# Performance work log

Measured on AMD Instinct MI355X. Metric: run time of the kernel, lower is better.

## Reference

```python
import jax, jax.numpy as jnp
import numpy as np

N = 100000
E = 2000000
F = 64          # in_features == out_features (required by attention * h_j)
BETA = 0.5
NEG_SLOPE = 0.01  # torch F.leaky_relu default


def setup_inputs() -> dict:
    key = jax.random.key(0)
    k1, k2, k3, k4, k5, k6 = jax.random.split(key, 6)
    h = jax.random.normal(k1, (N, F), dtype=jnp.float32)
    adj = jax.random.randint(k2, (2, E), 0, N, dtype=jnp.int64)
    amount = jax.random.uniform(k3, (E,), dtype=jnp.float32)
    count = jax.random.uniform(k4, (E,), dtype=jnp.float32)
    fc_w = jax.random.normal(k5, (F, 2 * F), dtype=jnp.float32) * (1.0 / np.sqrt(2 * F))
    fc_b = jax.random.normal(k6, (F,), dtype=jnp.float32) * 0.01
    return {"h": h, "adj": adj, "amount": amount, "count": count,
            "fc_w": fc_w, "fc_b": fc_b}


def _minmax_norm(x):
    lo, hi = x.min(), x.max()
    return (x - lo) / (hi - lo + 1e-8)


def reference(h, adj, amount, count, fc_w, fc_b):
    # per-edge weight from normalized amount/count
    edge_weight = BETA * _minmax_norm(amount) + (1.0 - BETA) * _minmax_norm(count)  # [E]

    src, dst = adj[0], adj[1]
    h_i = h[src]                     # [E, F]
    h_j = h[dst]                     # [E, F]
    h_cat = jnp.concatenate([h_i, h_j], axis=1)  # [E, 2F]

    score = jnp.einsum('ef,of->eo', h_cat, fc_w) + fc_b  # [E, F_out]
    score = jnp.where(score >= 0, score, NEG_SLOPE * score)  # leaky_relu
    score = score * edge_weight[:, None]

    # softmax over ALL edges (dim 0), per feature, as in the original
    attention = jax.nn.softmax(score, axis=0)  # [E, F]

    agg = jnp.zeros_like(h).at[src].add(attention * h_j)  # scatter-add -> [N, F]
    return agg
```

## Files before the change

kernel.cpp:

```cpp
#include <hip/hip_runtime.h>
#include <hip/hip_fp16.h>
#include <math.h>

#define FDIM   64
#define NB     64
#define BSHIFT 7
#define BMASK  127
#define EPTA   16
#define CHUNKA (EPTA * 256)
#define SCH    1024
#define DMASK  0xFFFFF

__global__ __launch_bounds__(256) void count_mm_k(const int* __restrict__ src,
                                                  const float* __restrict__ amount,
                                                  const float* __restrict__ count,
                                                  int* __restrict__ mat,
                                                  float4* __restrict__ partial,
                                                  double* __restrict__ colsum,
                                                  int E, int nblkA, int nbkt) {
  __shared__ int lhist[1024];
  __shared__ float4 lred[4];
  for (int k = threadIdx.x; k < nbkt; k += 256) lhist[k] = 0;
  if (blockIdx.x == 0)
    for (int i = threadIdx.x; i < 1024; i += 256) colsum[i] = 0.0;
  __syncthreads();
  float amin = 3.4e38f, amax = -3.4e38f, cmin = 3.4e38f, cmax = -3.4e38f;
  int e0 = blockIdx.x * CHUNKA + threadIdx.x * EPTA;
  if (e0 + EPTA <= E) {
    #pragma unroll
    for (int q = 0; q < EPTA; q += 4) {
      int4   s4 = *(const int4*)(src + e0 + q);
      float4 a4 = *(const float4*)(amount + e0 + q);
      float4 c4 = *(const float4*)(count + e0 + q);
      atomicAdd(&lhist[s4.x >> BSHIFT], 1);
      atomicAdd(&lhist[s4.y >> BSHIFT], 1);
      atomicAdd(&lhist[s4.z >> BSHIFT], 1);
      atomicAdd(&lhist[s4.w >> BSHIFT], 1);
      amin = fminf(amin, fminf(fminf(a4.x, a4.y), fminf(a4.z, a4.w)));
      amax = fmaxf(amax, fmaxf(fmaxf(a4.x, a4.y), fmaxf(a4.z, a4.w)));
      cmin = fminf(cmin, fminf(fminf(c4.x, c4.y), fminf(c4.z, c4.w)));
      cmax = fmaxf(cmax, fmaxf(fmaxf(c4.x, c4.y), fmaxf(c4.z, c4.w)));
    }
  } else {
    for (int e = e0; e < E; e++) {
      atomicAdd(&lhist[src[e] >> BSHIFT], 1);
      float a = amount[e], c = count[e];
      amin = fminf(amin, a); amax = fmaxf(amax, a);
      cmin = fminf(cmin, c); cmax = fmaxf(cmax, c);
    }
  }
  #pragma unroll
  for (int off = 32; off; off >>= 1) {
    amin = fminf(amin, __shfl_down(amin, off));
    amax = fmaxf(amax, __shfl_down(amax, off));
    cmin = fminf(cmin, __shfl_down(cmin, off));
    cmax = fmaxf(cmax, __shfl_down(cmax, off));
  }
  if ((threadIdx.x & 63) == 0) lred[threadIdx.x >> 6] = make_float4(amin, amax, cmin, cmax);
  __syncthreads();
  for (int k = threadIdx.x; k < nbkt; k += 256)
    mat[(size_t)k * nblkA + blockIdx.x] = lhist[k];
  if (threadIdx.x == 0) {
    float4 r = lred[0];
    #pragma unroll
    for (int w = 1; w < 4; w++) {
      r.x = fminf(r.x, lred[w].x); r.y = fmaxf(r.y, lred[w].y);
      r.z = fminf(r.z, lred[w].z); r.w = fmaxf(r.w, lred[w].w);
    }
    partial[blockIdx.x] = r;
  }
}

__global__ __launch_bounds__(256) void scan1_k(const int* __restrict__ v,
                                               int* __restrict__ bsum, int M) {
  __shared__ int lds[256];
  int t = threadIdx.x, b = blockIdx.x;
  int s = 0;
  for (int i = b * SCH + t; i < min((b + 1) * SCH, M); i += 256) s += v[i];
  lds[t] = s; __syncthreads();
  for (int off = 128; off; off >>= 1) {
    if (t < off) lds[t] += lds[t + off];
    __syncthreads();
  }
  if (t == 0) bsum[b] = lds[0];
}

__global__ __launch_bounds__(256) void scan2_k(const int* __restrict__ bsum,
                                               int* __restrict__ bexcl, int nchunk,
                                               const float4* __restrict__ partial,
                                               float* __restrict__ mmf, int nb) {
  __shared__ int lds[256];
  int t = threadIdx.x;
  int running = 0;
  for (int c0 = 0; c0 < nchunk; c0 += 256) {
    int x = (c0 + t < nchunk) ? bsum[c0 + t] : 0;
    lds[t] = x; __syncthreads();
    for (int off = 1; off < 256; off <<= 1) {
      int v = (t >= off) ? lds[t - off] : 0;
      __syncthreads();
      lds[t] += v; __syncthreads();
    }
    if (c0 + t < nchunk) bexcl[c0 + t] = running + lds[t] - x;
    running += lds[255];
    __syncthreads();
  }
  float amin = 3.4e38f, amax = -3.4e38f, cmin = 3.4e38f, cmax = -3.4e38f;
  for (int i = t; i < nb; i += 256) {
    float4 p = partial[i];
    amin = fminf(amin, p.x); amax = fmaxf(amax, p.y);
    cmin = fminf(cmin, p.z); cmax = fmaxf(cmax, p.w);
  }
  #pragma unroll
  for (int off = 32; off; off >>= 1) {
    amin = fminf(amin, __shfl_down(amin, off));
    amax = fmaxf(amax, __shfl_down(amax, off));
    cmin = fminf(cmin, __shfl_down(cmin, off));
    cmax = fmaxf(cmax, __shfl_down(cmax, off));
  }
  __shared__ float4 lred[4];
  if ((t & 63) == 0) lred[t >> 6] = make_float4(amin, amax, cmin, cmax);
  __syncthreads();
  if (t == 0) {
    float4 r = lred[0];
    #pragma unroll
    for (int w = 1; w < 4; w++) {
      r.x = fminf(r.x, lred[w].x); r.y = fmaxf(r.y, lred[w].y);
      r.z = fminf(r.z, lred[w].z); r.w = fmaxf(r.w, lred[w].w);
    }
    mmf[0] = r.x; mmf[1] = r.y; mmf[2] = r.z; mmf[3] = r.w;
  }
}

__global__ __launch_bounds__(256) void scan3_k(const int* __restrict__ v,
                                               const int* __restrict__ bexcl,
                                               int* __restrict__ smat, int M) {
  __shared__ int lds[256];
  int t = threadIdx.x, b = blockIdx.x;
  int running = bexcl[b];
  for (int tile = 0; tile < SCH; tile += 256) {
    int i = b * SCH + tile + t;
    int x = (i < M) ? v[i] : 0;
    lds[t] = x; __syncthreads();
    for (int off = 1; off < 256; off <<= 1) {
      int vv = (t >= off) ? lds[t - off] : 0;
      __syncthreads();
      lds[t] += vv; __syncthreads();
    }
    if (i < M) smat[i] = running + lds[t] - x;
    running += lds[255];
    __syncthreads();
  }
}

__global__ __launch_bounds__(256) void scatter_k(const int* __restrict__ src,
                                                 const int* __restrict__ dst,
                                                 const float* __restrict__ amount,
                                                 const float* __restrict__ count,
                                                 const float* __restrict__ mmf,
                                                 const int* __restrict__ smat,
                                                 int2* __restrict__ payload,
                                                 int E, int nblkA, int nbkt) {
  __shared__ int cntb[1024];
  __shared__ int baseb[1024];
  __shared__ int sbase[1024];
  __shared__ int wsum[4];
  __shared__ int2 lpay[CHUNKA];
  __shared__ unsigned short lbkt[CHUNKA];
  const int t = threadIdx.x, blk = blockIdx.x;
  for (int k = t; k < nbkt; k += 256) {
    cntb[k] = 0;
    sbase[k] = smat[(size_t)k * nblkA + blk];
  }
  __syncthreads();
  const float amin = mmf[0], amax = mmf[1], cmin = mmf[2], cmax = mmf[3];
  const float L2E = 1.4426950408889634f;
  const float ascale = 0.5f * L2E / (amax - amin + 1e-8f);
  const float cscale = 0.5f * L2E / (cmax - cmin + 1e-8f);
  int e0 = blk * CHUNKA + t * EPTA;
  const bool full = (e0 + EPTA <= E);
  int4 S[4]; int4 D[4]; float4 A[4]; float4 C[4];
  if (full) {
    #pragma unroll
    for (int q = 0; q < 4; q++) {
      S[q] = *(const int4*)(src + e0 + 4 * q);
      D[q] = *(const int4*)(dst + e0 + 4 * q);
      A[q] = *(const float4*)(amount + e0 + 4 * q);
      C[q] = *(const float4*)(count + e0 + 4 * q);
      atomicAdd(&cntb[S[q].x >> BSHIFT], 1);
      atomicAdd(&cntb[S[q].y >> BSHIFT], 1);
      atomicAdd(&cntb[S[q].z >> BSHIFT], 1);
      atomicAdd(&cntb[S[q].w >> BSHIFT], 1);
    }
  } else {
    for (int e = e0; e < E; e++) atomicAdd(&cntb[src[e] >> BSHIFT], 1);
  }
  __syncthreads();
  {
    const int wv = t >> 6, ln = t & 63;
    int carry = 0;
    #pragma unroll
    for (int c = 0; c < 4; c++) {
      int idx = (wv << 8) + (c << 6) + ln;
      int x = (idx < nbkt) ? cntb[idx] : 0;
      int v = x;
      #pragma unroll
      for (int off = 1; off < 64; off <<= 1) {
        int u = __shfl_up(v, off);
        if (ln >= off) v += u;
      }
      if (idx < nbkt) baseb[idx] = carry + v - x;
      carry += __shfl(v, 63);
    }
    if (ln == 0) wsum[wv] = carry;
  }
  __syncthreads();
  {
    const int wv = t >> 6, ln = t & 63;
    int wpre = 0;
    #pragma unroll
    for (int i = 0; i < 4; i++) wpre += (i < wv) ? wsum[i] : 0;
    if (wpre) {
      #pragma unroll
      for (int c = 0; c < 4; c++) {
        int idx = (wv << 8) + (c << 6) + ln;
        if (idx < nbkt) baseb[idx] += wpre;
      }
    }
  }
  __syncthreads();
  for (int k = t; k < nbkt; k += 256) cntb[k] = baseb[k];
  __syncthreads();
  auto ins = [&](int s, int d, float a, float c) {
    int b = s >> BSHIFT;
    float ew = (a - amin) * ascale + (c - cmin) * cscale;
    int pos = atomicAdd(&cntb[b], 1);
    lpay[pos] = make_int2(d | ((s & BMASK) << 20), __float_as_int(ew));
    lbkt[pos] = (unsigned short)b;
  };
  if (full) {
    #pragma unroll
    for (int q = 0; q < 4; q++) {
      ins(S[q].x, D[q].x, A[q].x, C[q].x);
      ins(S[q].y, D[q].y, A[q].y, C[q].y);
      ins(S[q].z, D[q].z, A[q].z, C[q].z);
      ins(S[q].w, D[q].w, A[q].w, C[q].w);
    }
  } else {
    for (int e = e0; e < E; e++) ins(src[e], dst[e], amount[e], count[e]);
  }
  __syncthreads();
  const int ned = min(CHUNKA, E - blk * CHUNKA);
  for (int i = t; i < ned; i += 256) {
    int bk = lbkt[i];
    payload[sbase[bk] + (i - baseb[bk])] = lpay[i];
  }
}

__global__ __launch_bounds__(512) void binB_k(const int2* __restrict__ payload,
                                              const int* __restrict__ smat,
                                              int2* __restrict__ edge_s,
                                              int E, int nblkA, int nbkt) {
  __shared__ int fcnt[128];
  __shared__ int fs[128];
  __shared__ int fcur[128];
  const int b = blockIdx.x;
  const int t = threadIdx.x;
  const int base = smat[(size_t)b * nblkA];
  const int end  = (b + 1 < nbkt) ? smat[(size_t)(b + 1) * nblkA] : E;
  if (t < 128) fcnt[t] = 0;
  __syncthreads();
  for (int i = base + t; i < end; i += 512)
    atomicAdd(&fcnt[payload[i].x >> 20], 1);
  __syncthreads();
  if (t < 128) fs[t] = fcnt[t];
  __syncthreads();
  for (int off = 1; off < 128; off <<= 1) {
    int v = 0;
    if (t < 128 && t >= off) v = fs[t - off];
    __syncthreads();
    if (t < 128) fs[t] += v;
    __syncthreads();
  }
  if (t < 128) fcur[t] = base + fs[t] - fcnt[t];
  __syncthreads();
  for (int i = base + t; i < end; i += 512) {
    int2 v = payload[i];
    int pos = atomicAdd(&fcur[v.x >> 20], 1);
    edge_s[pos] = v;
  }
}

__global__ __launch_bounds__(128) void pre_gemm(const float* __restrict__ h,
                                                const float* __restrict__ fc_w,
                                                const float* __restrict__ fc_b,
                                                float* __restrict__ G1,
                                                __half2* __restrict__ P, int N) {
  __shared__ float hs[NB * FDIM];
  const int t = threadIdx.x;
  const int o = t & 63, half = t >> 6;
  float w[FDIM];
  const float* wrow = fc_w + o * 128 + half * 64;
  #pragma unroll
  for (int f = 0; f < FDIM; f += 4) {
    float4 v = *(const float4*)(wrow + f);
    w[f] = v.x; w[f + 1] = v.y; w[f + 2] = v.z; w[f + 3] = v.w;
  }
  const float bias = (half == 0) ? fc_b[o] : 0.0f;
  const int n0 = blockIdx.x * NB;
  const int nrows = min(NB, N - n0);
  for (int i = t; i < nrows * FDIM; i += 128) hs[i] = h[(size_t)n0 * FDIM + i];
  __syncthreads();
  for (int n = 0; n < nrows; n++) {
    float4 a4 = make_float4(0.f, 0.f, 0.f, 0.f);
    #pragma unroll
    for (int f = 0; f < FDIM; f += 4) {
      float4 hv = *(const float4*)(&hs[n * FDIM + f]);
      a4.x += hv.x * w[f];
      a4.y += hv.y * w[f + 1];
      a4.z += hv.z * w[f + 2];
      a4.w += hv.w * w[f + 3];
    }
    float acc = (a4.x + a4.y) + (a4.z + a4.w) + bias;
    if (half == 0) {
      G1[(size_t)(n0 + n) * FDIM + o] = acc;
    } else {
      P[(size_t)(n0 + n) * FDIM + o] =
          __halves2half2(__float2half(acc), __float2half(hs[n * FDIM + o]));
    }
  }
}

__device__ __forceinline__ float2 unpack_h2(unsigned u) {
  __half2 v = *(__half2*)&u;
  return make_float2(__low2float(v), __high2float(v));
}

__global__ __launch_bounds__(256) void fused_k(const int2* __restrict__ edge_s,
                                               const int* __restrict__ smat,
                                               const float* __restrict__ G1,
                                               const unsigned* __restrict__ P,
                                               double* __restrict__ colsum,
                                               float* __restrict__ out,
                                               int E, int nblkA, int nbkt) {
  const int lane = threadIdx.x & 63;
  const int wv = __builtin_amdgcn_readfirstlane(threadIdx.x >> 6);
  const int wid = blockIdx.x * 4 + wv;
  const int nw = gridDim.x * 4;
  float csum = 0.0f;
  const int per = (((E + nw - 1) / nw) + 63) & ~63;
  const int e0 = wid * per;
  const int e1 = min(e0 + per, E);
  if (e0 < E) {
    int lo = 0, hi = nbkt - 1;
    while (lo < hi) {
      int mid = (lo + hi + 1) >> 1;
      if (smat[(size_t)mid * nblkA] <= e0) lo = mid; else hi = mid - 1;
    }
    int bkt = lo;
    int nextb = (bkt + 1 < nbkt) ? smat[(size_t)(bkt + 1) * nblkA] : E;
    int curnode = -1;
    bool firstf = true;
    float acc = 0.0f, g1 = 0.0f;
    auto flush_to = [&](int node) {
      if (curnode >= 0) {
        float* dp = out + (size_t)curnode * FDIM + lane;
        if (firstf) { atomicAdd(dp, acc); firstf = false; }
        else *dp = acc;
      }
      curnode = node; acc = 0.0f;
      g1 = G1[(size_t)node * FDIM + lane];
    };
    for (int c0 = e0; c0 < e1; c0 += 64) {
      const int m = min(64, e1 - c0);
      int2 p = make_int2(0, 0);
      if (lane < m) p = edge_s[c0 + lane];
      if (m == 64) {
        #pragma unroll 1
        for (int j = 0; j < 64; j += 16) {
          int dd[16], nd[16]; float ee[16]; unsigned uu[16];
          #pragma unroll
          for (int k = 0; k < 16; k++) {
            int x = __builtin_amdgcn_readlane(p.x, j + k);
            ee[k] = __int_as_float(__builtin_amdgcn_readlane(p.y, j + k));
            dd[k] = x & DMASK;
            nd[k] = x >> 20;
          }
          #pragma unroll
          for (int k = 0; k < 16; k++) uu[k] = P[(size_t)dd[k] * FDIM + lane];
          #pragma unroll
          for (int k = 0; k < 16; k++) {
            int i = c0 + j + k;
            while (i >= nextb) { bkt++; nextb = (bkt + 1 < nbkt) ? smat[(size_t)(bkt + 1) * nblkA] : E; }
            int node = (bkt << BSHIFT) + nd[k];
            if (node != curnode) flush_to(node);
            float2 v = unpack_h2(uu[k]);
            float sc = g1 + v.x;
            sc = fmaxf(sc, 0.01f * sc);
            float x = exp2f(sc * ee[k]);
            csum += x;
            acc += x * v.y;
          }
        }
      } else {
        for (int j = 0; j < m; j += 16) {
          const int rem = m - j;
          int dd[16], nd[16]; float ee[16]; unsigned uu[16];
          #pragma unroll
          for (int k = 0; k < 16; k++) {
            int x = __builtin_amdgcn_readlane(p.x, j + k);
            ee[k] = __int_as_float(__builtin_amdgcn_readlane(p.y, j + k));
            dd[k] = x & DMASK;
            nd[k] = x >> 20;
          }
          #pragma unroll
          for (int k = 0; k < 16; k++) uu[k] = P[(size_t)dd[k] * FDIM + lane];
          #pragma unroll
          for (int k = 0; k < 16; k++) {
            if (k < rem) {
              int i = c0 + j + k;
              while (i >= nextb) { bkt++; nextb = (bkt + 1 < nbkt) ? smat[(size_t)(bkt + 1) * nblkA] : E; }
              int node = (bkt << BSHIFT) + nd[k];
              if (node != curnode) flush_to(node);
              float2 v = unpack_h2(uu[k]);
              float sc = g1 + v.x;
              sc = fmaxf(sc, 0.01f * sc);
              float x = exp2f(sc * ee[k]);
              csum += x;
              acc += x * v.y;
            }
          }
        }
      }
    }
    if (curnode >= 0) atomicAdd(out + (size_t)curnode * FDIM + lane, acc);
  }
  __shared__ float part[256];
  part[threadIdx.x] = csum;
  __syncthreads();
  if (threadIdx.x < 64) {
    float tot = part[threadIdx.x] + part[threadIdx.x + 64] +
                part[threadIdx.x + 128] + part[threadIdx.x + 192];
    atomicAdd(&colsum[threadIdx.x * 16], (double)tot);
  }
}

__global__ __launch_bounds__(256) void scale_k(float4* __restrict__ out4,
                                               const double* __restrict__ colsum,
                                               int total4) {
  __shared__ float rinv_s[64];
  if (threadIdx.x < 64) rinv_s[threadIdx.x] = (float)(1.0 / colsum[threadIdx.x * 16]);
  __syncthreads();
  const float4* r4 = (const float4*)rinv_s;
  int idx = blockIdx.x * blockDim.x + threadIdx.x;
  int stride = gridDim.x * blockDim.x;
  for (int i = idx; i < total4; i += stride) {
    float4 v = out4[i];
    float4 r = r4[i & 15];
    v.x *= r.x; v.y *= r.y; v.z *= r.z; v.w *= r.w;
    out4[i] = v;
  }
}

extern "C" void kernel_launch(void* const* d_in, const int* in_sizes, int n_in,
                              void* d_out, int out_size, void* d_ws, size_t ws_size,
                              hipStream_t stream) {
  const float* h      = (const float*)d_in[0];
  const int*   adj    = (const int*)d_in[1];
  const float* amount = (const float*)d_in[2];
  const float* count  = (const float*)d_in[3];
  const float* fc_w   = (const float*)d_in[4];
  const float* fc_b   = (const float*)d_in[5];
  float* out = (float*)d_out;

  const int E = in_sizes[2];
  const int N = in_sizes[0] / FDIM;
  const int* src = adj;
  const int* dst = adj + E;
  const int nbkt  = (N + BMASK) >> BSHIFT;
  const int nblkA = (E + CHUNKA - 1) / CHUNKA;
  const int M = nbkt * nblkA;
  const int nchunk = (M + SCH - 1) / SCH;

  char* ws = (char*)d_ws;
  size_t off = 0;
  auto alloc = [&](size_t bytes) { void* p = ws + off; off += (bytes + 255) & ~(size_t)255; return p; };
  float*    G1      = (float*)alloc((size_t)N * FDIM * sizeof(float));
  __half2*  P       = (__half2*)alloc((size_t)N * FDIM * sizeof(__half2));
  int2*     edge_s  = (int2*)alloc((size_t)E * sizeof(int2));
  int2*     payload = (int2*)alloc((size_t)E * sizeof(int2));
  int*      mat     = (int*)alloc((size_t)M * sizeof(int));
  int*      smat    = (int*)alloc((size_t)M * sizeof(int));
  int*      bsum    = (int*)alloc((size_t)nchunk * sizeof(int));
  int*      bexcl   = (int*)alloc((size_t)nchunk * sizeof(int));
  float4*   mmpart  = (float4*)alloc((size_t)nblkA * sizeof(float4));
  double*   colsum  = (double*)alloc(1024 * sizeof(double));
  float*    mmf     = (float*)alloc(4 * sizeof(float));

  hipMemsetAsync(d_out, 0, (size_t)out_size * sizeof(float), stream);
  count_mm_k<<<nblkA, 256, 0, stream>>>(src, amount, count, mat, mmpart, colsum, E, nblkA, nbkt);
  scan1_k<<<nchunk, 256, 0, stream>>>(mat, bsum, M);
  scan2_k<<<1, 256, 0, stream>>>(bsum, bexcl, nchunk, mmpart, mmf, nblkA);
  scan3_k<<<nchunk, 256, 0, stream>>>(mat, bexcl, smat, M);
  scatter_k<<<nblkA, 256, 0, stream>>>(src, dst, amount, count, mmf, smat, payload, E, nblkA, nbkt);
  binB_k<<<nbkt, 512, 0, stream>>>(payload, smat, edge_s, E, nblkA, nbkt);
  pre_gemm<<<(N + NB - 1) / NB, 128, 0, stream>>>(h, fc_w, fc_b, G1, P, N);
  fused_k<<<4096, 256, 0, stream>>>(edge_s, smat, G1, (const unsigned*)P, colsum, out, E, nblkA, nbkt);
  scale_k<<<1024, 256, 0, stream>>>((float4*)out, colsum, N * FDIM / 4);
}
```

Before: 296.8 us.

## Fuse second-level bucket sort into the aggregation kernel via shared memory

Removes the separate binB_k pass that wrote a fully sorted edge array to global memory. Each 128-node bucket is now sorted by local source node in LDS inside the aggregation kernel, one block per bucket, in chunks of up to 3072 edges. The payload packing also changes so the destination index shifted by 8 is a byte offset into P, which drops the mask and multiply in the gather. The cost is a much smaller grid (one block per bucket), possible load imbalance, and atomics for every flush whenever a bucket spans several chunks.

```diff
diff --git a/kernel.cpp b/kernel.cpp
--- a/kernel.cpp
+++ b/kernel.cpp
@@ -9,7 +9,7 @@
 #define EPTA   16
 #define CHUNKA (EPTA * 256)
 #define SCH    1024
-#define DMASK  0xFFFFF
+#define CAP    3072
 
 __global__ __launch_bounds__(256) void count_mm_k(const int* __restrict__ src,
                                                   const float* __restrict__ amount,
@@ -234,7 +234,7 @@
     int b = s >> BSHIFT;
     float ew = (a - amin) * ascale + (c - cmin) * cscale;
     int pos = atomicAdd(&cntb[b], 1);
-    lpay[pos] = make_int2(d | ((s & BMASK) << 20), __float_as_int(ew));
+    lpay[pos] = make_int2((d << 8) | (s & BMASK), __float_as_int(ew));
     lbkt[pos] = (unsigned short)b;
   };
   if (full) {
@@ -253,40 +253,6 @@
   for (int i = t; i < ned; i += 256) {
     int bk = lbkt[i];
     payload[sbase[bk] + (i - baseb[bk])] = lpay[i];
-  }
-}
-
-__global__ __launch_bounds__(512) void binB_k(const int2* __restrict__ payload,
-                                              const int* __restrict__ smat,
-                                              int2* __restrict__ edge_s,
-                                              int E, int nblkA, int nbkt) {
-  __shared__ int fcnt[128];
-  __shared__ int fs[128];
-  __shared__ int fcur[128];
-  const int b = blockIdx.x;
-  const int t = threadIdx.x;
-  const int base = smat[(size_t)b * nblkA];
-  const int end  = (b + 1 < nbkt) ? smat[(size_t)(b + 1) * nblkA] : E;
-  if (t < 128) fcnt[t] = 0;
-  __syncthreads();
-  for (int i = base + t; i < end; i += 512)
-    atomicAdd(&fcnt[payload[i].x >> 20], 1);
-  __syncthreads();
-  if (t < 128) fs[t] = fcnt[t];
-  __syncthreads();
-  for (int off = 1; off < 128; off <<= 1) {
-    int v = 0;
-    if (t < 128 && t >= off) v = fs[t - off];
-    __syncthreads();
-    if (t < 128) fs[t] += v;
-    __syncthreads();
-  }
-  if (t < 128) fcur[t] = base + fs[t] - fcnt[t];
-  __syncthreads();
-  for (int i = base + t; i < end; i += 512) {
-    int2 v = payload[i];
-    int pos = atomicAdd(&fcur[v.x >> 20], 1);
-    edge_s[pos] = v;
   }
 }
 
@@ -335,63 +301,106 @@
   return make_float2(__low2float(v), __high2float(v));
 }
 
-__global__ __launch_bounds__(256) void fused_k(const int2* __restrict__ edge_s,
-                                               const int* __restrict__ smat,
-                                               const float* __restrict__ G1,
-                                               const unsigned* __restrict__ P,
-                                               double* __restrict__ colsum,
-                                               float* __restrict__ out,
-                                               int E, int nblkA, int nbkt) {
-  const int lane = threadIdx.x & 63;
-  const int wv = __builtin_amdgcn_readfirstlane(threadIdx.x >> 6);
-  const int wid = blockIdx.x * 4 + wv;
-  const int nw = gridDim.x * 4;
+__global__ __launch_bounds__(512) void fusedB_k(const int2* __restrict__ payload,
+                                                const int* __restrict__ smat,
+                                                const float* __restrict__ G1,
+                                                const unsigned* __restrict__ P,
+                                                double* __restrict__ colsum,
+                                                float* __restrict__ out,
+                                                int E, int nblkA, int nbkt) {
+  __shared__ int2 lpay[CAP];
+  __shared__ int fcnt[128];
+  __shared__ int fcur[128];
+  __shared__ float part[512];
+  const int b = blockIdx.x;
+  const int t = threadIdx.x;
+  const int lane = t & 63;
+  const int wv = __builtin_amdgcn_readfirstlane(t >> 6);
+  const int node0 = b << BSHIFT;
+  const int base = smat[(size_t)b * nblkA];
+  const int end  = (b + 1 < nbkt) ? smat[(size_t)(b + 1) * nblkA] : E;
+  const int nchunks = (end - base + CAP - 1) / CAP;
+  const bool multi = (nchunks > 1);
   float csum = 0.0f;
-  const int per = (((E + nw - 1) / nw) + 63) & ~63;
-  const int e0 = wid * per;
-  const int e1 = min(e0 + per, E);
-  if (e0 < E) {
-    int lo = 0, hi = nbkt - 1;
-    while (lo < hi) {
-      int mid = (lo + hi + 1) >> 1;
-      if (smat[(size_t)mid * nblkA] <= e0) lo = mid; else hi = mid - 1;
-    }
-    int bkt = lo;
-    int nextb = (bkt + 1 < nbkt) ? smat[(size_t)(bkt + 1) * nblkA] : E;
+  for (int c = 0; c < nchunks; c++) {
+    const int cs = base + c * CAP;
+    const int m = min(CAP, end - cs);
+    if (t < 128) fcnt[t] = 0;
+    __syncthreads();
+    int2 myp0, myp1, myp2, myp3, myp4, myp5;
+    {
+      int i;
+      i = t;            if (i < m) { myp0 = payload[cs + i]; atomicAdd(&fcnt[myp0.x & 127], 1); }
+      i = t + 512;      if (i < m) { myp1 = payload[cs + i]; atomicAdd(&fcnt[myp1.x & 127], 1); }
+      i = t + 1024;     if (i < m) { myp2 = payload[cs + i]; atomicAdd(&fcnt[myp2.x & 127], 1); }
+      i = t + 1536;     if (i < m) { myp3 = payload[cs + i]; atomicAdd(&fcnt[myp3.x & 127], 1); }
+      i = t + 2048;     if (i < m) { myp4 = payload[cs + i]; atomicAdd(&fcnt[myp4.x & 127], 1); }
+      i = t + 2560;     if (i < m) { myp5 = payload[cs + i]; atomicAdd(&fcnt[myp5.x & 127], 1); }
+    }
+    __syncthreads();
+    if (wv == 0) {
+      int carry = 0;
+      #pragma unroll
+      for (int cc = 0; cc < 2; cc++) {
+        int idx = (cc << 6) + lane;
+        int x = fcnt[idx];
+        int v = x;
+        #pragma unroll
+        for (int off = 1; off < 64; off <<= 1) {
+          int u = __shfl_up(v, off);
+          if (lane >= off) v += u;
+        }
+        fcur[idx] = carry + v - x;
+        carry += __shfl(v, 63);
+      }
+    }
+    __syncthreads();
+    {
+      int i;
+      i = t;            if (i < m) lpay[atomicAdd(&fcur[myp0.x & 127], 1)] = myp0;
+      i = t + 512;      if (i < m) lpay[atomicAdd(&fcur[myp1.x & 127], 1)] = myp1;
+      i = t + 1024;     if (i < m) lpay[atomicAdd(&fcur[myp2.x & 127], 1)] = myp2;
+      i = t + 1536;     if (i < m) lpay[atomicAdd(&fcur[myp3.x & 127], 1)] = myp3;
+      i = t + 2048;     if (i < m) lpay[atomicAdd(&fcur[myp4.x & 127], 1)] = myp4;
+      i = t + 2560;     if (i < m) lpay[atomicAdd(&fcur[myp5.x & 127], 1)] = myp5;
+    }
+    __syncthreads();
+    const int per = (((m + 7) >> 3) + 63) & ~63;
+    const int ws = wv * per;
+    const int we = min(ws + per, m);
     int curnode = -1;
     bool firstf = true;
     float acc = 0.0f, g1 = 0.0f;
     auto flush_to = [&](int node) {
       if (curnode >= 0) {
         float* dp = out + (size_t)curnode * FDIM + lane;
-        if (firstf) { atomicAdd(dp, acc); firstf = false; }
+        if (multi || firstf) { atomicAdd(dp, acc); firstf = false; }
         else *dp = acc;
       }
       curnode = node; acc = 0.0f;
       g1 = G1[(size_t)node * FDIM + lane];
     };
-    for (int c0 = e0; c0 < e1; c0 += 64) {
-      const int m = min(64, e1 - c0);
+    for (int c0 = ws; c0 < we; c0 += 64) {
+      const int mm = min(64, we - c0);
       int2 p = make_int2(0, 0);
-      if (lane < m) p = edge_s[c0 + lane];
-      if (m == 64) {
+      if (lane < mm) p = lpay[c0 + lane];
+      if (mm == 64) {
         #pragma unroll 1
         for (int j = 0; j < 64; j += 16) {
-          int dd[16], nd[16]; float ee[16]; unsigned uu[16];
+          int xs[16]; float ee[16]; unsigned uu[16];
           #pragma unroll
           for (int k = 0; k < 16; k++) {
-            int x = __builtin_amdgcn_readlane(p.x, j + k);
+            xs[k] = __builtin_amdgcn_readlane(p.x, j + k);
             ee[k] = __int_as_float(__builtin_amdgcn_readlane(p.y, j + k));
-            dd[k] = x & DMASK;
-            nd[k] = x >> 20;
           }
           #pragma unroll
-          for (int k = 0; k < 16; k++) uu[k] = P[(size_t)dd[k] * FDIM + lane];
+          for (int k = 0; k < 16; k++) {
+            unsigned off = (((unsigned)xs[k]) & 0xFFFFFF00u) | ((unsigned)lane << 2);
+            uu[k] = *(const unsigned*)((const char*)P + off);
+          }
           #pragma unroll
           for (int k = 0; k < 16; k++) {
-            int i = c0 + j + k;
-            while (i >= nextb) { bkt++; nextb = (bkt + 1 < nbkt) ? smat[(size_t)(bkt + 1) * nblkA] : E; }
-            int node = (bkt << BSHIFT) + nd[k];
+            int node = node0 + (xs[k] & 127);
             if (node != curnode) flush_to(node);
             float2 v = unpack_h2(uu[k]);
             float sc = g1 + v.x;
@@ -402,24 +411,23 @@
           }
         }
       } else {
-        for (int j = 0; j < m; j += 16) {
-          const int rem = m - j;
-          int dd[16], nd[16]; float ee[16]; unsigned uu[16];
+        for (int j = 0; j < mm; j += 16) {
+          const int rem = mm - j;
+          int xs[16]; float ee[16]; unsigned uu[16];
           #pragma unroll
           for (int k = 0; k < 16; k++) {
-            int x = __builtin_amdgcn_readlane(p.x, j + k);
+            xs[k] = __builtin_amdgcn_readlane(p.x, j + k);
             ee[k] = __int_as_float(__builtin_amdgcn_readlane(p.y, j + k));
-            dd[k] = x & DMASK;
-            nd[k] = x >> 20;
           }
           #pragma unroll
-          for (int k = 0; k < 16; k++) uu[k] = P[(size_t)dd[k] * FDIM + lane];
+          for (int k = 0; k < 16; k++) {
+            unsigned off = (((unsigned)xs[k]) & 0xFFFFFF00u) | ((unsigned)lane << 2);
+            uu[k] = *(const unsigned*)((const char*)P + off);
+          }
           #pragma unroll
           for (int k = 0; k < 16; k++) {
             if (k < rem) {
-              int i = c0 + j + k;
-              while (i >= nextb) { bkt++; nextb = (bkt + 1 < nbkt) ? smat[(size_t)(bkt + 1) * nblkA] : E; }
-              int node = (bkt << BSHIFT) + nd[k];
+              int node = node0 + (xs[k] & 127);
               if (node != curnode) flush_to(node);
               float2 v = unpack_h2(uu[k]);
               float sc = g1 + v.x;
@@ -434,13 +442,13 @@
     }
     if (curnode >= 0) atomicAdd(out + (size_t)curnode * FDIM + lane, acc);
   }
-  __shared__ float part[256];
-  part[threadIdx.x] = csum;
-  __syncthreads();
-  if (threadIdx.x < 64) {
-    float tot = part[threadIdx.x] + part[threadIdx.x + 64] +
-                part[threadIdx.x + 128] + part[threadIdx.x + 192];
-    atomicAdd(&colsum[threadIdx.x * 16], (double)tot);
+  part[t] = csum;
+  __syncthreads();
+  if (t < 64) {
+    float tot = 0.0f;
+    #pragma unroll
+    for (int w = 0; w < 8; w++) tot += part[t + (w << 6)];
+    atomicAdd(&colsum[t * 16], (double)tot);
   }
 }
 
@@ -486,7 +494,6 @@
   auto alloc = [&](size_t bytes) { void* p = ws + off; off += (bytes + 255) & ~(size_t)255; return p; };
   float*    G1      = (float*)alloc((size_t)N * FDIM * sizeof(float));
   __half2*  P       = (__half2*)alloc((size_t)N * FDIM * sizeof(__half2));
-  int2*     edge_s  = (int2*)alloc((size_t)E * sizeof(int2));
   int2*     payload = (int2*)alloc((size_t)E * sizeof(int2));
   int*      mat     = (int*)alloc((size_t)M * sizeof(int));
   int*      smat    = (int*)alloc((size_t)M * sizeof(int));
@@ -502,8 +509,7 @@
   scan2_k<<<1, 256, 0, stream>>>(bsum, bexcl, nchunk, mmpart, mmf, nblkA);
   scan3_k<<<nchunk, 256, 0, stream>>>(mat, bexcl, smat, M);
   scatter_k<<<nblkA, 256, 0, stream>>>(src, dst, amount, count, mmf, smat, payload, E, nblkA, nbkt);
-  binB_k<<<nbkt, 512, 0, stream>>>(payload, smat, edge_s, E, nblkA, nbkt);
   pre_gemm<<<(N + NB - 1) / NB, 128, 0, stream>>>(h, fc_w, fc_b, G1, P, N);
-  fused_k<<<4096, 256, 0, stream>>>(edge_s, smat, G1, (const unsigned*)P, colsum, out, E, nblkA, nbkt);
+  fusedB_k<<<nbkt, 512, 0, stream>>>(payload, smat, G1, (const unsigned*)P, colsum, out, E, nblkA, nbkt);
   scale_k<<<1024, 256, 0, stream>>>((float4*)out, colsum, N * FDIM / 4);
 }
```

Result: no change. 291.3 us (-1.8%).
